# Kernel tuning notes

Measured on AMD Instinct MI355X. Metric: run time of the kernel, lower is better.

## Reference

```python
import jax, jax.numpy as jnp
import numpy as np

KH = KW = 3
K = KH * KW
OG = 1  # offset_groups
WG = 1  # weight_groups
DIL = 1

def _conv_same(x, w):
    # stride-1 SAME NCHW conv, matching the keras offset/mask convs
    return jax.lax.conv_general_dilated(
        x, w, window_strides=(1, 1), padding='SAME',
        dimension_numbers=('NCHW', 'OIHW', 'NCHW'))

def _deform_conv2d(x, w, offset, mask):
    # x: [B,C,H,W]; w: [F, C//WG, KH, KW]
    # offset: [B, OG*2*K, H, W] laid out as (og, k, {dy,dx});
    # mask:   [B, OG*K, H, W]
    B, C, H, W = x.shape
    F = w.shape[0]
    pad_h = ((KH - 1) * DIL) // 2
    pad_w = ((KW - 1) * DIL) // 2
    ky = jnp.arange(KH) * DIL - pad_h
    kx = jnp.arange(KW) * DIL - pad_w
    kyy, kxx = jnp.meshgrid(ky, kx, indexing='ij')
    kyy = kyy.reshape(K).astype(x.dtype)
    kxx = kxx.reshape(K).astype(x.dtype)

    off = offset.reshape(B, OG, K, 2, H, W)
    dy = off[:, :, :, 0]  # [B,OG,K,H,W]
    dx = off[:, :, :, 1]
    oy = jnp.arange(H, dtype=x.dtype)
    ox = jnp.arange(W, dtype=x.dtype)
    y = oy[None, None, None, :, None] + kyy[None, None, :, None, None] + dy
    xq = ox[None, None, None, None, :] + kxx[None, None, :, None, None] + dx

    y0 = jnp.floor(y)
    x0 = jnp.floor(xq)
    wy = y - y0   # [B,OG,K,H,W]
    wx = xq - x0
    y0i = y0.astype(jnp.int32)
    x0i = x0.astype(jnp.int32)

    Cg = C // OG
    xg = x.reshape(B, OG, Cg, H * W)

    def gather(yi, xi):
        valid = (yi >= 0) & (yi < H) & (xi >= 0) & (xi < W)
        idx = jnp.clip(yi, 0, H - 1) * W + jnp.clip(xi, 0, W - 1)
        flat = idx.reshape(B, OG, 1, K * H * W)
        v = jnp.take_along_axis(xg, flat, axis=3)   # [B,OG,Cg,K*H*W]
        v = v.reshape(B, OG, Cg, K, H, W)
        return v * valid[:, :, None].astype(x.dtype)

    v00 = gather(y0i, x0i)
    v01 = gather(y0i, x0i + 1)
    v10 = gather(y0i + 1, x0i)
    v11 = gather(y0i + 1, x0i + 1)
    wy_ = wy[:, :, None]
    wx_ = wx[:, :, None]
    samp = (v00 * (1 - wy_) * (1 - wx_) + v01 * (1 - wy_) * wx_
            + v10 * wy_ * (1 - wx_) + v11 * wy_ * wx_)  # [B,OG,Cg,K,H,W]
    m = mask.reshape(B, OG, K, H, W)[:, :, None]
    samp = samp * m
    wr = w.reshape(F, OG, Cg, K)
    return jnp.einsum('bgckhw,fgck->bfhw', samp, wr)


def setup_inputs() -> dict:
    key = jax.random.key(0)
    k1, k2, k3, k4 = jax.random.split(key, 4)
    B, C, H, W = 8, 256, 64, 64
    F = 256
    x = jax.random.normal(k1, (B, C, H, W), dtype=jnp.float32)
    w_offset = jax.random.normal(k2, (OG * 2 * K, C, KH, KW), dtype=jnp.float32) * 0.01
    w_mask = jax.random.normal(k3, (OG * K, C, KH, KW), dtype=jnp.float32) * 0.01
    w_deform = jax.random.normal(k4, (F, C // WG, KH, KW), dtype=jnp.float32) * 0.05
    return {'x': x, 'w_offset': w_offset, 'w_mask': w_mask, 'w_deform': w_deform}


def reference(x, w_offset, w_mask, w_deform):
    offset = _conv_same(x, w_offset)                 # [B, 2K, H, W]
    mask = jax.nn.sigmoid(_conv_same(x, w_mask))     # [B, K, H, W]
    return _deform_conv2d(x, w_deform, offset, mask)
```

## Files before the change

kernel.cpp:

```cpp
#include <hip/hip_runtime.h>
#include <hip/hip_bf16.h>
#include <hip/hip_fp16.h>
#include <math.h>

constexpr int Bn = 8, Cn = 256, Hn = 64, Wn = 64, Fn = 256, Kn = 9;
constexpr int HWn = Hn * Wn;
constexpr int NM = Bn * Kn * HWn;
constexpr int NCH = 4;

using frag_ab = __attribute__((ext_vector_type(8))) short;
using frag_h  = __attribute__((ext_vector_type(8))) _Float16;
using f32x4   = __attribute__((ext_vector_type(4))) float;

__device__ inline ushort f2bf(float f) {
    union { float f; uint32_t u; } un{f};
    return (ushort)((un.u + 0x7FFF + ((un.u >> 16) & 1)) >> 16);
}
__device__ inline ushort f2h(float f) {
    __half h = __float2half_rn(f);
    return *reinterpret_cast<ushort*>(&h);
}

__global__ __launch_bounds__(256) void wtrans2(const float* __restrict__ wd,
                                               ushort* __restrict__ wB) {
    int i = blockIdx.x * 256 + threadIdx.x;
    if (i >= Fn * Cn * Kn) return;
    int ci = i & 7, fi = (i >> 3) & 15, G = (i >> 7) & 31, ft = (i >> 12) & 15, k = i >> 16;
    int f = ft * 16 + fi, c = G * 8 + ci;
    wB[i] = f2h(wd[(f * Cn + c) * 9 + k]);
}

__global__ __launch_bounds__(256) void wpack27(const float* __restrict__ wo,
                                               const float* __restrict__ wm,
                                               ushort* __restrict__ wA) {
    int i = blockIdx.x * 256 + threadIdx.x;
    if (i >= 73728) return;
    int ci = i & 7, l = (i >> 3) & 63, mt = (i >> 9) & 1, cblk = (i >> 10) & 7, tap = i >> 13;
    int m = mt * 16 + (l & 15);
    int c = cblk * 32 + ((l >> 4) & 3) * 8 + ci;
    float v = 0.f;
    if (m < 18)      v = wo[(m * Cn + c) * 9 + tap];
    else if (m < 27) v = wm[((m - 18) * Cn + c) * 9 + tap];
    wA[i] = f2bf(v);
}

__global__ __launch_bounds__(256) void xpose(const float* __restrict__ x,
                                             __half2* __restrict__ xh) {
    int i = blockIdx.x * 256 + threadIdx.x;
    int p = i & 4095, q = (i >> 12) & 3, b = i >> 14;
    const float* xp = x + (size_t)b * Cn * HWn + p;
    __half2* op = xh + (((size_t)b * 4096 + p) << 7) + q * 32;
#pragma unroll
    for (int j = 0; j < 32; ++j) {
        int c = q * 64 + 2 * j;
        op[j] = __float22half2_rn(make_float2(xp[(size_t)c * HWn],
                                              xp[(size_t)(c + 1) * HWn]));
    }
}

__global__ __launch_bounds__(256) void offconv27(const float* __restrict__ x,
                                                 const ushort* __restrict__ wA,
                                                 float* __restrict__ part) {
    __shared__ ushort xs[4][66][40];
    const int t = threadIdx.x;
    const int l = t & 63, w = t >> 6;
    const int li = l & 15, lg = l >> 4;
    const int rb = blockIdx.x, ch = blockIdx.y, b = blockIdx.z;
    const int h0 = rb * 2;
    const int rw = w >> 1, pt0 = (w & 1) * 2;

    f32x4 acc[2][2];
#pragma unroll
    for (int mt = 0; mt < 2; ++mt)
#pragma unroll
        for (int q = 0; q < 2; ++q) acc[mt][q] = (f32x4)0.f;

    const float* xb = x + (size_t)b * Cn * HWn;

#pragma unroll 1
    for (int cc = 0; cc < 2; ++cc) {
        const int cbase = ch * 64 + cc * 32;
        __syncthreads();
        for (int j = t; j < 1056; j += 256) {
            int cq = j / 264;
            int rem = j - cq * 264;
            int r = rem / 66, col = rem - r * 66;
            int rg = h0 - 1 + r, cg = col - 1;
            ushort u[8];
            if ((unsigned)rg < (unsigned)Hn && (unsigned)cg < (unsigned)Wn) {
                const float* xp = xb + (size_t)(cbase + cq * 8) * HWn + (rg << 6) + cg;
#pragma unroll
                for (int jj = 0; jj < 8; ++jj) u[jj] = f2bf(xp[(size_t)jj * HWn]);
            } else {
#pragma unroll
                for (int jj = 0; jj < 8; ++jj) u[jj] = 0;
            }
            *(int4*)&xs[r][col][cq * 8] =
                make_int4(u[0] | (u[1] << 16), u[2] | (u[3] << 16),
                          u[4] | (u[5] << 16), u[6] | (u[7] << 16));
        }
        __syncthreads();
        const int cblk = ch * 2 + cc;
#pragma unroll
        for (int tap = 0; tap < 9; ++tap) {
            const int ky = tap / 3, kx = tap - 3 * (tap / 3);
            frag_ab a0 = *(const frag_ab*)(wA + (size_t)((tap * 8 + cblk) * 2) * 512 + l * 8);
            frag_ab a1 = *(const frag_ab*)(wA + (size_t)((tap * 8 + cblk) * 2 + 1) * 512 + l * 8);
#pragma unroll
            for (int q = 0; q < 2; ++q) {
                frag_ab bf = *(const frag_ab*)&xs[rw + ky][(pt0 + q) * 16 + li + kx][lg * 8];
                acc[0][q] = __builtin_amdgcn_mfma_f32_16x16x32_bf16(a0, bf, acc[0][q], 0, 0, 0);
                acc[1][q] = __builtin_amdgcn_mfma_f32_16x16x32_bf16(a1, bf, acc[1][q], 0, 0, 0);
            }
        }
    }

    const int h = h0 + rw;
#pragma unroll
    for (int mt = 0; mt < 2; ++mt)
#pragma unroll
        for (int j = 0; j < 4; ++j) {
            int m = mt * 16 + lg * 4 + j;
            if (m < 27) {
#pragma unroll
                for (int q = 0; q < 2; ++q) {
                    int pixel = (pt0 + q) * 16 + li;
                    part[((size_t)((ch * Bn + b) * 27 + m) << 12) + (h << 6) + pixel] =
                        acc[mt][q][j];
                }
            }
        }
}

__global__ __launch_bounds__(256) void metafin9(const float* __restrict__ part,
                                                int4* __restrict__ mpack) {
    const int k = blockIdx.y;
    const int idx = blockIdx.x * 256 + threadIdx.x;
    const int b = idx >> 12, p = idx & 4095;
    const int h = p >> 6, w = p & 63;

    float dy = 0.f, dx = 0.f, ms = 0.f;
#pragma unroll
    for (int ch = 0; ch < NCH; ++ch) {
        size_t base = ((size_t)((ch * Bn + b) * 27) << 12) + p;
        dy += part[base + ((size_t)(2 * k) << 12)];
        dx += part[base + ((size_t)(2 * k + 1) << 12)];
        ms += part[base + ((size_t)(18 + k) << 12)];
    }
    float m = 1.f / (1.f + expf(-ms));
    float yy = (float)(h + k / 3 - 1) + dy;
    float xx = (float)(w + k % 3 - 1) + dx;
    float y0f = floorf(yy), x0f = floorf(xx);
    float wy = yy - y0f, wx = xx - x0f;
    int y0 = (int)y0f, x0 = (int)x0f;
    int y1 = y0 + 1, x1 = x0 + 1;
    bool vy0 = (unsigned)y0 < (unsigned)Hn;
    bool vx0 = (unsigned)x0 < (unsigned)Wn;
    bool vy1 = (unsigned)y1 < (unsigned)Hn;
    bool vx1 = (unsigned)x1 < (unsigned)Wn;
    int cy0 = min(max(y0, 0), Hn - 1), cx0 = min(max(x0, 0), Wn - 1);
    int cy1 = min(max(y1, 0), Hn - 1), cx1 = min(max(x1, 0), Wn - 1);
    float w00 = (vy0 && vx0) ? (1.f - wy) * (1.f - wx) * m : 0.f;
    float w01 = (vy0 && vx1) ? (1.f - wy) * wx * m : 0.f;
    float w10 = (vy1 && vx0) ? wy * (1.f - wx) * m : 0.f;
    float w11 = (vy1 && vx1) ? wy * wx * m : 0.f;
    int i00 = (cy0 << 6) + cx0, i01 = (cy0 << 6) + cx1;
    int i10 = (cy1 << 6) + cx0, i11 = (cy1 << 6) + cx1;
    union { struct { __half a, bh; } h; int i; } pz, pw;
    pz.h.a = __float2half_rn(w00); pz.h.bh = __float2half_rn(w01);
    pw.h.a = __float2half_rn(w10); pw.h.bh = __float2half_rn(w11);
    int q = ((b * 9 + k) << 12) + p;
    mpack[q] = make_int4(i00 | (i01 << 16), i10 | (i11 << 16), pz.i, pw.i);
}

__global__ __launch_bounds__(512, 4) void dconv(const __half2* __restrict__ xh,
                                                const ushort* __restrict__ wB,
                                                const int4* __restrict__ mpack,
                                                float* __restrict__ out) {
    __shared__ ushort sl[2][64][64];
    const int t = threadIdx.x;
    const int l = t & 63, w = t >> 6;
    const int li = l & 15, lg = l >> 4;
    const int hl = l >> 5;
    const int cl = l & 31;
    const int b = blockIdx.x;
    const int p0 = blockIdx.y << 6;

    f32x4 acc[2][4];
#pragma unroll
    for (int a = 0; a < 2; ++a)
#pragma unroll
        for (int q = 0; q < 4; ++q) acc[a][q] = (f32x4)0.f;

    int4 m4[4];
    const __half2* xb = xh + (((size_t)b) << 19);

    auto LOADMETA = [&](int k) {
#pragma unroll
        for (int u = 0; u < 4; ++u) {
            int pix = w * 8 + 2 * u + hl;
            m4[u] = mpack[((b * 9 + k) << 12) + p0 + pix];
        }
    };

    auto STAGE = [&](int s, int buf) {
        const int ch = s & 3;
        const int co = ch * 32 + cl;
#pragma unroll
        for (int u = 0; u < 4; ++u) {
            int i00 = m4[u].x & 0xFFFF, i01 = ((unsigned)m4[u].x) >> 16;
            int i10 = m4[u].y & 0xFFFF, i11 = ((unsigned)m4[u].y) >> 16;
            union { int i; __half2 h; } uz, uw;
            uz.i = m4[u].z; uw.i = m4[u].w;
            __half2 v00 = xb[i00 * 128 + co];
            __half2 v01 = xb[i01 * 128 + co];
            __half2 v10 = xb[i10 * 128 + co];
            __half2 v11 = xb[i11 * 128 + co];
            __half2 sum = __hmul2(__half2half2(__low2half(uz.h)), v00);
            sum = __hfma2(__half2half2(__high2half(uz.h)), v01, sum);
            sum = __hfma2(__half2half2(__low2half(uw.h)), v10, sum);
            sum = __hfma2(__half2half2(__high2half(uw.h)), v11, sum);
            int pix = w * 8 + 2 * u + hl;
            int slot = (cl >> 2) ^ (pix & 7);
            *(__half2*)&sl[buf][pix][(slot << 3) + ((cl & 3) << 1)] = sum;
        }
    };

    auto COMPUTE = [&](int s, int buf) {
        const int k = s >> 2, ch = s & 3;
        const ushort* wp = wB + ((size_t)((k * 16 + 2 * w) * 512 + ch * 128)) * 8;
#pragma unroll
        for (int h = 0; h < 2; ++h) {
            frag_h bq[4];
#pragma unroll
            for (int pt = 0; pt < 4; ++pt)
                bq[pt] = *(const frag_h*)&sl[buf][pt * 16 + li]
                                           [((((h << 2) | lg) ^ (l & 7)) << 3)];
#pragma unroll
            for (int ft = 0; ft < 2; ++ft) {
                frag_h a = *(const frag_h*)(wp + (size_t)(ft * 512 + h * 64 + l) * 8);
#pragma unroll
                for (int pt = 0; pt < 4; ++pt)
                    acc[ft][pt] = __builtin_amdgcn_mfma_f32_16x16x32_f16(
                        a, bq[pt], acc[ft][pt], 0, 0, 0);
            }
        }
    };

    LOADMETA(0);
    STAGE(0, 0);
    __syncthreads();
#pragma unroll 1
    for (int s = 0; s < 36; ++s) {
        const int cur = s & 1;
        if (s + 1 < 36) {
            if (((s + 1) & 3) == 0) LOADMETA((s + 1) >> 2);
            STAGE(s + 1, cur ^ 1);
        }
        COMPUTE(s, cur);
        __syncthreads();
    }

    float* ob = out + (size_t)b * Fn * HWn + p0;
#pragma unroll
    for (int ft = 0; ft < 2; ++ft)
#pragma unroll
        for (int j = 0; j < 4; ++j) {
            int f = w * 32 + ft * 16 + lg * 4 + j;
#pragma unroll
            for (int pt = 0; pt < 4; ++pt)
                ob[(size_t)f * HWn + pt * 16 + li] = acc[ft][pt][j];
        }
}

extern "C" void kernel_launch(void* const* d_in, const int* in_sizes, int n_in,
                              void* d_out, int out_size, void* d_ws, size_t ws_size,
                              hipStream_t stream) {
    const float* x  = (const float*)d_in[0];
    const float* wo = (const float*)d_in[1];
    const float* wm = (const float*)d_in[2];
    const float* wd = (const float*)d_in[3];
    float* out = (float*)d_out;

    int4*    mpack = (int4*)d_ws;
    char*    region = (char*)d_ws + (size_t)NM * 16;
    float*   part  = (float*)region;
    ushort*  wBp   = (ushort*)region;
    __half2* xh    = (__half2*)(region + 1179648);
    ushort*  wA27  = (ushort*)(region + 18874368);

    wpack27<<<dim3(288), dim3(256), 0, stream>>>(wo, wm, wA27);
    offconv27<<<dim3(32, NCH, Bn), dim3(256), 0, stream>>>(x, wA27, part);
    metafin9<<<dim3(Bn * HWn / 256, 9), dim3(256), 0, stream>>>(part, mpack);
    wtrans2<<<dim3((Fn * Cn * Kn + 255) / 256), dim3(256), 0, stream>>>(wd, wBp);
    xpose<<<dim3(Bn * 4 * HWn / 256), dim3(256), 0, stream>>>(x, xh);
    dconv<<<dim3(Bn, HWn / 64), dim3(512), 0, stream>>>(xh, wBp, mpack, out);
}
```

Measured before the change: 113.3 us.

## Restructure deform-conv staging into finer channel steps with LDS-cached sampling metadata

```diff
diff --git a/kernel.cpp b/kernel.cpp
--- a/kernel.cpp
+++ b/kernel.cpp
@@ -173,16 +173,17 @@
     mpack[q] = make_int4(i00 | (i01 << 16), i10 | (i11 << 16), pz.i, pw.i);
 }
 
-__global__ __launch_bounds__(512, 4) void dconv(const __half2* __restrict__ xh,
+__global__ __launch_bounds__(512, 4) void dconv(const uint32_t* __restrict__ xh,
                                                 const ushort* __restrict__ wB,
                                                 const int4* __restrict__ mpack,
                                                 float* __restrict__ out) {
-    __shared__ ushort sl[2][64][64];
+    __shared__ uint32_t sl[2][64][20];
+    __shared__ int4 ml[9][64];
     const int t = threadIdx.x;
     const int l = t & 63, w = t >> 6;
     const int li = l & 15, lg = l >> 4;
-    const int hl = l >> 5;
-    const int cl = l & 31;
+    const int pu = (w << 3) + (l >> 3);
+    const int g  = l & 7;
     const int b = blockIdx.x;
     const int p0 = blockIdx.y << 6;
 
@@ -192,71 +193,65 @@
 #pragma unroll
         for (int q = 0; q < 4; ++q) acc[a][q] = (f32x4)0.f;
 
-    int4 m4[4];
-    const __half2* xb = xh + (((size_t)b) << 19);
-
-    auto LOADMETA = [&](int k) {
-#pragma unroll
-        for (int u = 0; u < 4; ++u) {
-            int pix = w * 8 + 2 * u + hl;
-            m4[u] = mpack[((b * 9 + k) << 12) + p0 + pix];
-        }
+    const uint32_t* xb = xh + ((size_t)b << 19);
+
+    for (int j = t; j < 576; j += 512)
+        ml[j >> 6][j & 63] = mpack[((b * 9 + (j >> 6)) << 12) + p0 + (j & 63)];
+    __syncthreads();
+
+    auto STAGE = [&](int s, int buf) {
+        const int k = s % 9, ch = s / 9;
+        const int4 m = ml[k][pu];
+        const int i00 = m.x & 0xFFFF, i01 = ((unsigned)m.x) >> 16;
+        const int i10 = m.y & 0xFFFF, i11 = ((unsigned)m.y) >> 16;
+        union { int i; __half2 h; } uz, uw;
+        uz.i = m.z; uw.i = m.w;
+        const uint32_t* base = xb + (ch << 4) + (g << 1);
+        uint2 v00 = *(const uint2*)(base + i00 * 128);
+        uint2 v01 = *(const uint2*)(base + i01 * 128);
+        uint2 v10 = *(const uint2*)(base + i10 * 128);
+        uint2 v11 = *(const uint2*)(base + i11 * 128);
+        const __half2 w00 = __half2half2(__low2half(uz.h));
+        const __half2 w01 = __half2half2(__high2half(uz.h));
+        const __half2 w10 = __half2half2(__low2half(uw.h));
+        const __half2 w11 = __half2half2(__high2half(uw.h));
+        __half2 r0 = __hmul2(w00, *(__half2*)&v00.x);
+        r0 = __hfma2(w01, *(__half2*)&v01.x, r0);
+        r0 = __hfma2(w10, *(__half2*)&v10.x, r0);
+        r0 = __hfma2(w11, *(__half2*)&v11.x, r0);
+        __half2 r1 = __hmul2(w00, *(__half2*)&v00.y);
+        r1 = __hfma2(w01, *(__half2*)&v01.y, r1);
+        r1 = __hfma2(w10, *(__half2*)&v10.y, r1);
+        r1 = __hfma2(w11, *(__half2*)&v11.y, r1);
+        uint2 rr;
+        rr.x = *(uint32_t*)&r0;
+        rr.y = *(uint32_t*)&r1;
+        *(uint2*)&sl[buf][pu][g << 1] = rr;
     };
 
-    auto STAGE = [&](int s, int buf) {
-        const int ch = s & 3;
-        const int co = ch * 32 + cl;
-#pragma unroll
-        for (int u = 0; u < 4; ++u) {
-            int i00 = m4[u].x & 0xFFFF, i01 = ((unsigned)m4[u].x) >> 16;
-            int i10 = m4[u].y & 0xFFFF, i11 = ((unsigned)m4[u].y) >> 16;
-            union { int i; __half2 h; } uz, uw;
-            uz.i = m4[u].z; uw.i = m4[u].w;
-            __half2 v00 = xb[i00 * 128 + co];
-            __half2 v01 = xb[i01 * 128 + co];
-            __half2 v10 = xb[i10 * 128 + co];
-            __half2 v11 = xb[i11 * 128 + co];
-            __half2 sum = __hmul2(__half2half2(__low2half(uz.h)), v00);
-            sum = __hfma2(__half2half2(__high2half(uz.h)), v01, sum);
-            sum = __hfma2(__half2half2(__low2half(uw.h)), v10, sum);
-            sum = __hfma2(__half2half2(__high2half(uw.h)), v11, sum);
-            int pix = w * 8 + 2 * u + hl;
-            int slot = (cl >> 2) ^ (pix & 7);
-            *(__half2*)&sl[buf][pix][(slot << 3) + ((cl & 3) << 1)] = sum;
+    auto COMPUTE = [&](int s, int buf) {
+        const int k = s % 9, ch = s / 9;
+        frag_h bq[4];
+#pragma unroll
+        for (int pt = 0; pt < 4; ++pt)
+            bq[pt] = *(const frag_h*)&sl[buf][pt * 16 + li][lg << 2];
+#pragma unroll
+        for (int ft = 0; ft < 2; ++ft) {
+            frag_h a = *(const frag_h*)(wB + (((size_t)(k * 16 + 2 * w + ft)) << 12)
+                                           + (ch << 9) + (l << 3));
+#pragma unroll
+            for (int pt = 0; pt < 4; ++pt)
+                acc[ft][pt] = __builtin_amdgcn_mfma_f32_16x16x32_f16(
+                    a, bq[pt], acc[ft][pt], 0, 0, 0);
         }
     };
 
-    auto COMPUTE = [&](int s, int buf) {
-        const int k = s >> 2, ch = s & 3;
-        const ushort* wp = wB + ((size_t)((k * 16 + 2 * w) * 512 + ch * 128)) * 8;
-#pragma unroll
-        for (int h = 0; h < 2; ++h) {
-            frag_h bq[4];
-#pragma unroll
-            for (int pt = 0; pt < 4; ++pt)
-                bq[pt] = *(const frag_h*)&sl[buf][pt * 16 + li]
-                                           [((((h << 2) | lg) ^ (l & 7)) << 3)];
-#pragma unroll
-            for (int ft = 0; ft < 2; ++ft) {
-                frag_h a = *(const frag_h*)(wp + (size_t)(ft * 512 + h * 64 + l) * 8);
-#pragma unroll
-                for (int pt = 0; pt < 4; ++pt)
-                    acc[ft][pt] = __builtin_amdgcn_mfma_f32_16x16x32_f16(
-                        a, bq[pt], acc[ft][pt], 0, 0, 0);
-            }
-        }
-    };
-
-    LOADMETA(0);
     STAGE(0, 0);
     __syncthreads();
 #pragma unroll 1
-    for (int s = 0; s < 36; ++s) {
+    for (int s = 0; s < 72; ++s) {
         const int cur = s & 1;
-        if (s + 1 < 36) {
-            if (((s + 1) & 3) == 0) LOADMETA((s + 1) >> 2);
-            STAGE(s + 1, cur ^ 1);
-        }
+        if (s + 1 < 72) STAGE(s + 1, cur ^ 1);
         COMPUTE(s, cur);
         __syncthreads();
     }
@@ -282,17 +277,18 @@
     const float* wd = (const float*)d_in[3];
     float* out = (float*)d_out;
 
-    int4*    mpack = (int4*)d_ws;
-    char*    region = (char*)d_ws + (size_t)NM * 16;
-    float*   part  = (float*)region;
-    ushort*  wBp   = (ushort*)region;
-    __half2* xh    = (__half2*)(region + 1179648);
-    ushort*  wA27  = (ushort*)(region + 18874368);
+    int4*     mpack = (int4*)d_ws;
+    char*     region = (char*)d_ws + (size_t)NM * 16;
+    float*    part  = (float*)region;
+    ushort*   wBp   = (ushort*)region;
+    __half2*  xhh   = (__half2*)(region + 1179648);
+    uint32_t* xhu   = (uint32_t*)(region + 1179648);
+    ushort*   wA27  = (ushort*)(region + 18874368);
 
     wpack27<<<dim3(288), dim3(256), 0, stream>>>(wo, wm, wA27);
     offconv27<<<dim3(32, NCH, Bn), dim3(256), 0, stream>>>(x, wA27, part);
     metafin9<<<dim3(Bn * HWn / 256, 9), dim3(256), 0, stream>>>(part, mpack);
     wtrans2<<<dim3((Fn * Cn * Kn + 255) / 256), dim3(256), 0, stream>>>(wd, wBp);
-    xpose<<<dim3(Bn * 4 * HWn / 256), dim3(256), 0, stream>>>(x, xh);
-    dconv<<<dim3(Bn, HWn / 64), dim3(512), 0, stream>>>(xh, wBp, mpack, out);
-}
+    xpose<<<dim3(Bn * 4 * HWn / 256), dim3(256), 0, stream>>>(x, xhh);
+    dconv<<<dim3(Bn, HWn / 64), dim3(512), 0, stream>>>(xhu, wBp, mpack, out);
+}
```

Result: slower. 118.7 us (+4.8%).
